# Kernel optimization log

Hardware: AMD Instinct MI355X
Metric: run time of the kernel (lower is better)

The kernel has to match this reference:

```python
import jax, jax.numpy as jnp
import numpy as np

N = 20000
E = 640000
IN_DIM = 128
HID = 128
OUT = 64


def setup_inputs() -> dict:
    key = jax.random.key(0)
    ks = jax.random.split(key, 16)
    s = 0.05
    inp = {
        'feat': jax.random.normal(ks[0], (N, IN_DIM), jnp.float32),
        'edge_index': jax.random.randint(ks[1], (2, E), 0, N, jnp.int64),
        # GCNConv params
        'W_gcn': jax.random.normal(ks[2], (IN_DIM, HID), jnp.float32) * s,
        'b_gcn': jnp.zeros((HID,), jnp.float32),
        # SAGEConv params (lin_l: aggregated neighbors w/ bias; lin_r: root, no bias)
        'W_sage_l': jax.random.normal(ks[3], (HID, HID), jnp.float32) * s,
        'b_sage_l': jnp.zeros((HID,), jnp.float32),
        'W_sage_r': jax.random.normal(ks[4], (HID, HID), jnp.float32) * s,
        # policy MLP
        'W1': jax.random.normal(ks[5], (HID, HID), jnp.float32) * s,
        'b1': jnp.zeros((HID,), jnp.float32),
        'W2': jax.random.normal(ks[6], (HID, HID), jnp.float32) * s,
        'b2': jnp.zeros((HID,), jnp.float32),
        'W3': jax.random.normal(ks[7], (HID, OUT), jnp.float32) * s,
        'b3': jnp.zeros((OUT,), jnp.float32),
        # value head
        'Wv': jax.random.normal(ks[8], (HID, 1), jnp.float32) * s,
        'bv': jnp.zeros((1,), jnp.float32),
    }
    return inp


def _gcn(feat, src, dst, W, b):
    # PyG GCNConv: add self loops, sym-normalize by deg^-1/2 on both ends
    loop = jnp.arange(N, dtype=src.dtype)
    s = jnp.concatenate([src, loop])
    d = jnp.concatenate([dst, loop])
    deg = jax.ops.segment_sum(jnp.ones_like(d, jnp.float32), d, num_segments=N)
    dinv = jnp.where(deg > 0, jax.lax.rsqrt(deg), 0.0)
    x = feat @ W  # [N, HID]
    msg = x[s] * (dinv[s] * dinv[d])[:, None]  # [E+N, HID]
    return jax.ops.segment_sum(msg, d, num_segments=N) + b


def _sage_mean(h, src, dst, Wl, bl, Wr):
    # PyG SAGEConv(aggr='mean'): lin_l(mean_neigh) + lin_r(root)
    neigh_sum = jax.ops.segment_sum(h[src], dst, num_segments=N)
    cnt = jax.ops.segment_sum(jnp.ones_like(dst, jnp.float32), dst, num_segments=N)
    mean = neigh_sum / jnp.maximum(cnt, 1.0)[:, None]
    return mean @ Wl + bl + h @ Wr


def reference(feat, edge_index, W_gcn, b_gcn, W_sage_l, b_sage_l, W_sage_r,
              W1, b1, W2, b2, W3, b3, Wv, bv):
    src, dst = edge_index[0], edge_index[1]
    h = jax.nn.relu(_gcn(feat, src, dst, W_gcn, b_gcn))
    h = jax.nn.relu(_sage_mean(h, src, dst, W_sage_l, b_sage_l, W_sage_r))
    # policy MLP (GELU exact, matching torch nn.GELU default)
    z = jax.nn.gelu(h @ W1 + b1, approximate=False)
    z = jax.nn.gelu(z @ W2 + b2, approximate=False)
    means = z @ W3 + b3  # [N, OUT]
    values = (h @ Wv + bv)[:, 0]  # [N]
    return (means, values)
```

## Files before the change

kernel.cpp:

```cpp
#include <hip/hip_runtime.h>
#include <math.h>


typedef __attribute__((ext_vector_type(8))) short short8;
typedef __attribute__((ext_vector_type(4))) float floatx4;

__device__ __forceinline__ unsigned short f2b(float f) {
    unsigned u = __float_as_uint(f);
    unsigned r = (u + 0x7fffu + ((u >> 16) & 1u)) >> 16;
    return (unsigned short)r;
}
__device__ __forceinline__ float b2f_lo(unsigned v) {
    return __uint_as_float(v << 16);
}
__device__ __forceinline__ float b2f_hi(unsigned v) {
    return __uint_as_float(v & 0xffff0000u);
}
__device__ __forceinline__ floatx4 MFMA(short8 a, short8 b, floatx4 c) {
    return __builtin_amdgcn_mfma_f32_16x16x32_bf16(a, b, c, 0, 0, 0);
}
__device__ __forceinline__ float gelu_exact(float x) {
    return 0.5f * x * (1.0f + erff(x * 0.70710678118654752440f));
}

#define FRAG(P, ct, ks, lane) (*(const short8*)((P) + (((((ct)*4 + (ks))*64) + (lane)) << 3)))


__global__ __launch_bounds__(256) void count_pack_kernel(
    const int* __restrict__ eidx, int E, int* __restrict__ cnt,
    const float* Wg, const float* Wsl, const float* Wsr,
    const float* W1, const float* W2, const float* W3,
    unsigned short* Pg, unsigned short* Psl, unsigned short* Psr,
    unsigned short* P1, unsigned short* P2, unsigned short* P3,
    int countBlocks)
{
    if ((int)blockIdx.x < countBlocks) {
        int e = blockIdx.x * 256 + threadIdx.x;
        if (e < E) atomicAdd(&cnt[eidx[E + e]], 1);
        return;
    }
    int t = (blockIdx.x - countBlocks) * 256 + threadIdx.x;
    const float* W; unsigned short* P; int NC = 128; int base;
    if (t < 2048)       { W = Wg;  P = Pg;  base = t; }
    else if (t < 4096)  { W = Wsl; P = Psl; base = t - 2048; }
    else if (t < 6144)  { W = Wsr; P = Psr; base = t - 4096; }
    else if (t < 8192)  { W = W1;  P = P1;  base = t - 6144; }
    else if (t < 10240) { W = W2;  P = P2;  base = t - 8192; }
    else if (t < 11264) { W = W3;  P = P3;  base = t - 10240; NC = 64; }
    else return;
    int l  = base & 63;
    int ks = (base >> 6) & 3;
    int ct = base >> 8;
    int n  = ct * 16 + (l & 15);
    int k0 = ks * 32 + ((l >> 4) << 3);
    short8 v;
    #pragma unroll
    for (int j = 0; j < 8; j++) v[j] = (short)f2b(W[(size_t)(k0 + j) * NC + n]);
    *(short8*)(P + ((size_t)base << 3)) = v;
}


__global__ __launch_bounds__(256) void scan_kernel(
    const int* __restrict__ cnt, int N,
    int* __restrict__ row_ptr, int* __restrict__ wptr, float* __restrict__ dinv,
    int* __restrict__ gflags, int* __restrict__ gsums)
{
    __shared__ int sh[256];
    __shared__ int s_off;
    int b = blockIdx.x, tid = threadIdx.x;
    int i0 = b * 1024 + tid * 4;
    int v0 = (i0 + 0 < N) ? cnt[i0 + 0] : 0;
    int v1 = (i0 + 1 < N) ? cnt[i0 + 1] : 0;
    int v2 = (i0 + 2 < N) ? cnt[i0 + 2] : 0;
    int v3 = (i0 + 3 < N) ? cnt[i0 + 3] : 0;
    int tot = v0 + v1 + v2 + v3;
    sh[tid] = tot;
    __syncthreads();
    for (int off = 1; off < 256; off <<= 1) {
        int t = (tid >= off) ? sh[tid - off] : 0;
        __syncthreads();
        sh[tid] += t;
        __syncthreads();
    }
    if (tid == 255) {
        gsums[b] = sh[255];
        __hip_atomic_store(&gflags[b], 1, __ATOMIC_RELEASE, __HIP_MEMORY_SCOPE_AGENT);
    }
    if (tid == 0) {
        int off = 0;
        for (int j = 0; j < b; j++) {
            while (__hip_atomic_load(&gflags[j], __ATOMIC_ACQUIRE,
                                     __HIP_MEMORY_SCOPE_AGENT) == 0) {}
            off += gsums[j];
        }
        s_off = off;
    }
    __syncthreads();
    int excl = s_off + sh[tid] - tot;
    if (i0 + 0 < N) { row_ptr[i0 + 0] = excl;                wptr[i0 + 0] = excl;                dinv[i0 + 0] = rsqrtf((float)(v0 + 1)); }
    if (i0 + 1 < N) { row_ptr[i0 + 1] = excl + v0;           wptr[i0 + 1] = excl + v0;           dinv[i0 + 1] = rsqrtf((float)(v1 + 1)); }
    if (i0 + 2 < N) { row_ptr[i0 + 2] = excl + v0 + v1;      wptr[i0 + 2] = excl + v0 + v1;      dinv[i0 + 2] = rsqrtf((float)(v2 + 1)); }
    if (i0 + 3 < N) { row_ptr[i0 + 3] = excl + v0 + v1 + v2; wptr[i0 + 3] = excl + v0 + v1 + v2; dinv[i0 + 3] = rsqrtf((float)(v3 + 1)); }
    if (b == (int)gridDim.x - 1 && tid == 255) row_ptr[N] = s_off + sh[255];
}


__global__ __launch_bounds__(256) void fill_gemm_kernel(
    const int* __restrict__ eidx, int E, int N,
    int* __restrict__ wptr, int* __restrict__ col,
    const float* __restrict__ feat, const float* __restrict__ dinv,
    const unsigned short* __restrict__ Pg, unsigned short* __restrict__ xs,
    int M, int fillBlocks, int PS)
{
    if ((int)blockIdx.x < fillBlocks) {
        int p = blockIdx.x & 7;
        int chunk = blockIdx.x >> 3;
        int dlo = p * PS;
        int dhi = dlo + PS; if (dhi > N) dhi = N;
        #pragma unroll
        for (int it = 0; it < 8; it++) {
            int e = (chunk * 8 + it) * 256 + threadIdx.x;
            if (e < E) {
                int d = eidx[E + e];
                if (d >= dlo && d < dhi) {
                    int pos = atomicAdd(&wptr[d], 1);
                    col[pos] = eidx[e];
                }
            }
        }
        return;
    }
    int bid = blockIdx.x - fillBlocks;
    int w = bid * 4 + (threadIdx.x >> 6);
    if (w >= (M / 16) * 2) return;
    int lane = threadIdx.x & 63;
    int m = lane & 15, quad = lane >> 4;
    int rt = w >> 1, ch = w & 1;
    const float* arow = feat + (size_t)(rt * 16 + m) * 128;
    short8 a[4];
    #pragma unroll
    for (int ks = 0; ks < 4; ks++) {
        float4 f0 = *(const float4*)(arow + ks * 32 + quad * 8);
        float4 f1 = *(const float4*)(arow + ks * 32 + quad * 8 + 4);
        short8 s;
        s[0] = (short)f2b(f0.x); s[1] = (short)f2b(f0.y);
        s[2] = (short)f2b(f0.z); s[3] = (short)f2b(f0.w);
        s[4] = (short)f2b(f1.x); s[5] = (short)f2b(f1.y);
        s[6] = (short)f2b(f1.z); s[7] = (short)f2b(f1.w);
        a[ks] = s;
    }
    float dvr[4];
    #pragma unroll
    for (int reg = 0; reg < 4; reg++) dvr[reg] = dinv[rt * 16 + quad * 4 + reg];
    #pragma unroll
    for (int ct = 0; ct < 4; ct++) {
        floatx4 acc = {0.f, 0.f, 0.f, 0.f};
        #pragma unroll
        for (int ks = 0; ks < 4; ks++)
            acc = MFMA(a[ks], FRAG(Pg, ch * 4 + ct, ks, lane), acc);
        #pragma unroll
        for (int reg = 0; reg < 4; reg++)
            xs[(size_t)(rt * 16 + quad * 4 + reg) * 128 + (ch * 4 + ct) * 16 + m] =
                f2b(acc[reg] * dvr[reg]);
    }
}


#define ACCUM(q)                                   \
    acc[0] += b2f_lo((q).x); acc[1] += b2f_hi((q).x); \
    acc[2] += b2f_lo((q).y); acc[3] += b2f_hi((q).y); \
    acc[4] += b2f_lo((q).z); acc[5] += b2f_hi((q).z); \
    acc[6] += b2f_lo((q).w); acc[7] += b2f_hi((q).w);

template<bool GCN>
__global__ __launch_bounds__(256) void agg_kernel(
    const unsigned short* __restrict__ X, const int* __restrict__ row_ptr,
    const int* __restrict__ col, const float* __restrict__ dinv,
    const float* __restrict__ bias, unsigned short* __restrict__ Y, int N)
{
    int w = (int)((blockIdx.x * 256 + threadIdx.x) >> 6);
    if (w >= N) return;
    int lane = threadIdx.x & 63;
    int g = lane >> 4, t = lane & 15;
    const uint4* Xq = (const uint4*)X;
    int beg = row_ptr[w], end = row_ptr[w + 1];
    int deg = end - beg;

    float acc[8] = {0.f, 0.f, 0.f, 0.f, 0.f, 0.f, 0.f, 0.f};
    int jb = beg;
    for (; jb + 16 <= end; jb += 16) {
        int s0 = col[jb + g];
        int s1 = col[jb + g + 4];
        int s2 = col[jb + g + 8];
        int s3 = col[jb + g + 12];
        uint4 q0 = Xq[(size_t)s0 * 16 + t];
        uint4 q1 = Xq[(size_t)s1 * 16 + t];
        uint4 q2 = Xq[(size_t)s2 * 16 + t];
        uint4 q3 = Xq[(size_t)s3 * 16 + t];
        ACCUM(q0) ACCUM(q1) ACCUM(q2) ACCUM(q3)
    }
    for (; jb < end; jb += 4) {
        int j = jb + g;
        if (j < end) {
            int s = col[j];
            uint4 q = Xq[(size_t)s * 16 + t];
            ACCUM(q)
        }
    }
    #pragma unroll
    for (int i = 0; i < 8; i++) {
        acc[i] += __shfl_xor(acc[i], 16);
        acc[i] += __shfl_xor(acc[i], 32);
    }
    if (g == 0) {
        float out[8];
        if (GCN) {
            uint4 q = Xq[(size_t)w * 16 + t];
            ACCUM(q)
            float dw = dinv[w];
            float4 b0 = *(const float4*)(bias + t * 8);
            float4 b1 = *(const float4*)(bias + t * 8 + 4);
            out[0] = fmaxf(fmaf(acc[0], dw, b0.x), 0.f);
            out[1] = fmaxf(fmaf(acc[1], dw, b0.y), 0.f);
            out[2] = fmaxf(fmaf(acc[2], dw, b0.z), 0.f);
            out[3] = fmaxf(fmaf(acc[3], dw, b0.w), 0.f);
            out[4] = fmaxf(fmaf(acc[4], dw, b1.x), 0.f);
            out[5] = fmaxf(fmaf(acc[5], dw, b1.y), 0.f);
            out[6] = fmaxf(fmaf(acc[6], dw, b1.z), 0.f);
            out[7] = fmaxf(fmaf(acc[7], dw, b1.w), 0.f);
        } else {
            float rc = 1.0f / (float)(deg > 0 ? deg : 1);
            #pragma unroll
            for (int i = 0; i < 8; i++) out[i] = acc[i] * rc;
        }
        uint4 r;
        r.x = (unsigned)f2b(out[0]) | ((unsigned)f2b(out[1]) << 16);
        r.y = (unsigned)f2b(out[2]) | ((unsigned)f2b(out[3]) << 16);
        r.z = (unsigned)f2b(out[4]) | ((unsigned)f2b(out[5]) << 16);
        r.w = (unsigned)f2b(out[6]) | ((unsigned)f2b(out[7]) << 16);
        ((uint4*)Y)[(size_t)w * 16 + t] = r;
    }
}


__global__ __launch_bounds__(256) void sage_mlp_kernel(
    const unsigned short* __restrict__ mean, const unsigned short* __restrict__ h1,
    const unsigned short* __restrict__ Psl, const unsigned short* __restrict__ Psr,
    const float* __restrict__ bsl,
    const unsigned short* __restrict__ P1, const float* __restrict__ b1,
    const unsigned short* __restrict__ P2, const float* __restrict__ b2,
    const unsigned short* __restrict__ P3, const float* __restrict__ b3,
    const float* __restrict__ Wv, const float* __restrict__ bv,
    float* __restrict__ means, float* __restrict__ values, int M)
{
    __shared__ unsigned short z[4][16 * 136];
    int widx = threadIdx.x >> 6, lane = threadIdx.x & 63;
    int w = blockIdx.x * 4 + widx;
    if (w >= M / 16) return;
    int m = lane & 15, quad = lane >> 4;
    unsigned short* zt = &z[widx][0];
    int r0 = w * 16;

    short8 am[4], ar[4];
    #pragma unroll
    for (int ks = 0; ks < 4; ks++) {
        am[ks] = *(const short8*)(mean + (size_t)(r0 + m) * 128 + ks * 32 + quad * 8);
        ar[ks] = *(const short8*)(h1   + (size_t)(r0 + m) * 128 + ks * 32 + quad * 8);
    }

    float vpart[4] = {0.f, 0.f, 0.f, 0.f};
    #pragma unroll
    for (int ct = 0; ct < 8; ct++) {
        floatx4 acc = {0.f, 0.f, 0.f, 0.f};
        #pragma unroll
        for (int ks = 0; ks < 4; ks++) acc = MFMA(am[ks], FRAG(Psl, ct, ks, lane), acc);
        #pragma unroll
        for (int ks = 0; ks < 4; ks++) acc = MFMA(ar[ks], FRAG(Psr, ct, ks, lane), acc);
        float bb = bsl[ct * 16 + m];
        float wv = Wv[ct * 16 + m];
        #pragma unroll
        for (int reg = 0; reg < 4; reg++) {
            float o = fmaxf(acc[reg] + bb, 0.f);
            vpart[reg] = fmaf(o, wv, vpart[reg]);
            zt[(quad * 4 + reg) * 136 + ct * 16 + m] = f2b(o);
        }
    }
    #pragma unroll
    for (int off = 1; off <= 8; off <<= 1) {
        #pragma unroll
        for (int reg = 0; reg < 4; reg++)
            vpart[reg] += __shfl_xor(vpart[reg], off);
    }
    if (m == 0) {
        float bvv = bv[0];
        #pragma unroll
        for (int reg = 0; reg < 4; reg++)
            values[r0 + quad * 4 + reg] = vpart[reg] + bvv;
    }

    short8 a1[4];
    #pragma unroll
    for (int ks = 0; ks < 4; ks++)
        a1[ks] = *(const short8*)(zt + m * 136 + ks * 32 + quad * 8);

    #pragma unroll
    for (int ct = 0; ct < 8; ct++) {
        floatx4 acc = {0.f, 0.f, 0.f, 0.f};
        #pragma unroll
        for (int ks = 0; ks < 4; ks++) acc = MFMA(a1[ks], FRAG(P1, ct, ks, lane), acc);
        float bb = b1[ct * 16 + m];
        #pragma unroll
        for (int reg = 0; reg < 4; reg++)
            zt[(quad * 4 + reg) * 136 + ct * 16 + m] = f2b(gelu_exact(acc[reg] + bb));
    }
    short8 a2[4];
    #pragma unroll
    for (int ks = 0; ks < 4; ks++)
        a2[ks] = *(const short8*)(zt + m * 136 + ks * 32 + quad * 8);

    #pragma unroll
    for (int ct = 0; ct < 8; ct++) {
        floatx4 acc = {0.f, 0.f, 0.f, 0.f};
        #pragma unroll
        for (int ks = 0; ks < 4; ks++) acc = MFMA(a2[ks], FRAG(P2, ct, ks, lane), acc);
        float bb = b2[ct * 16 + m];
        #pragma unroll
        for (int reg = 0; reg < 4; reg++)
            zt[(quad * 4 + reg) * 136 + ct * 16 + m] = f2b(gelu_exact(acc[reg] + bb));
    }
    short8 a3[4];
    #pragma unroll
    for (int ks = 0; ks < 4; ks++)
        a3[ks] = *(const short8*)(zt + m * 136 + ks * 32 + quad * 8);

    #pragma unroll
    for (int ct = 0; ct < 4; ct++) {
        floatx4 acc = {0.f, 0.f, 0.f, 0.f};
        #pragma unroll
        for (int ks = 0; ks < 4; ks++) acc = MFMA(a3[ks], FRAG(P3, ct, ks, lane), acc);
        float bb = b3[ct * 16 + m];
        #pragma unroll
        for (int reg = 0; reg < 4; reg++)
            means[(size_t)(r0 + quad * 4 + reg) * 64 + ct * 16 + m] = acc[reg] + bb;
    }
}


extern "C" void kernel_launch(void* const* d_in, const int* in_sizes, int n_in,
                              void* d_out, int out_size, void* d_ws, size_t ws_size,
                              hipStream_t stream) {
    const float* feat  = (const float*)d_in[0];
    const int*   eidx  = (const int*)d_in[1];
    const float* W_gcn = (const float*)d_in[2];
    const float* b_gcn = (const float*)d_in[3];
    const float* W_sl  = (const float*)d_in[4];
    const float* b_sl  = (const float*)d_in[5];
    const float* W_sr  = (const float*)d_in[6];
    const float* W1    = (const float*)d_in[7];
    const float* b1    = (const float*)d_in[8];
    const float* W2    = (const float*)d_in[9];
    const float* b2    = (const float*)d_in[10];
    const float* W3    = (const float*)d_in[11];
    const float* b3    = (const float*)d_in[12];
    const float* Wv    = (const float*)d_in[13];
    const float* bv    = (const float*)d_in[14];

    const int N = in_sizes[0] / 128;
    const int E = in_sizes[1] / 2;

    char* ws = (char*)d_ws;
    size_t off = 0;
    auto alloc = [&](size_t bytes) -> void* {
        void* p = ws + off;
        off += (bytes + 255) & ~(size_t)255;
        return p;
    };
    int*   gflags  = (int*)alloc((size_t)(64 + N) * 4);
    int*   cnt     = gflags + 64;
    size_t zbytes  = (size_t)(64 + N) * 4;
    int*   gsums   = (int*)alloc(64 * 4);
    int*   row_ptr = (int*)alloc((size_t)(N + 1) * 4);
    int*   wptr    = (int*)alloc((size_t)N * 4);
    float* dinv    = (float*)alloc((size_t)N * 4);
    int*   col     = (int*)alloc((size_t)E * 4);
    unsigned short* xs   = (unsigned short*)alloc((size_t)N * 128 * 2);
    unsigned short* h1   = (unsigned short*)alloc((size_t)N * 128 * 2);
    unsigned short* mean = (unsigned short*)alloc((size_t)N * 128 * 2);
    unsigned short* Pg   = (unsigned short*)alloc(2048 * 8 * 2);
    unsigned short* Psl  = (unsigned short*)alloc(2048 * 8 * 2);
    unsigned short* Psr  = (unsigned short*)alloc(2048 * 8 * 2);
    unsigned short* P1   = (unsigned short*)alloc(2048 * 8 * 2);
    unsigned short* P2   = (unsigned short*)alloc(2048 * 8 * 2);
    unsigned short* P3   = (unsigned short*)alloc(1024 * 8 * 2);

    hipMemsetAsync(gflags, 0, zbytes, stream);

    const int countBlocks = (E + 255) / 256;
    const int packBlocks  = (11264 + 255) / 256;
    count_pack_kernel<<<countBlocks + packBlocks, 256, 0, stream>>>(
        eidx, E, cnt, W_gcn, W_sl, W_sr, W1, W2, W3,
        Pg, Psl, Psr, P1, P2, P3, countBlocks);

    const int NB = (N + 1023) / 1024;
    scan_kernel<<<NB, 256, 0, stream>>>(cnt, N, row_ptr, wptr, dinv, gflags, gsums);

    const int PS = (N + 7) / 8;
    const int chunks = (E + 2047) / 2048;
    const int fillBlocks = chunks * 8;
    const int gemmBlocks = ((N / 16) * 2 + 3) / 4;
    fill_gemm_kernel<<<fillBlocks + gemmBlocks, 256, 0, stream>>>(
        eidx, E, N, wptr, col, feat, dinv, Pg, xs, N, fillBlocks, PS);

    const int agrid = (N + 3) / 4;
    agg_kernel<true><<<agrid, 256, 0, stream>>>(xs, row_ptr, col, dinv, b_gcn, h1, N);
    agg_kernel<false><<<agrid, 256, 0, stream>>>(h1, row_ptr, col, dinv, nullptr, mean, N);

    sage_mlp_kernel<<<(N / 16 + 3) / 4, 256, 0, stream>>>(
        mean, h1, Psl, Psr, b_sl, P1, b1, P2, b2, P3, b3, Wv, bv,
        (float*)d_out, (float*)d_out + (size_t)N * 64, N);
}
```

Measured before the change: 221.0 us.

## Record per-edge rank during counting and restructure aggregation to two nodes per wave

Result: slower. 253.7 us (+14.8%).

```diff
diff --git a/kernel.cpp b/kernel.cpp
--- a/kernel.cpp
+++ b/kernel.cpp
@@ -7,27 +7,25 @@
 
 __device__ __forceinline__ unsigned short f2b(float f) {
     unsigned u = __float_as_uint(f);
-    unsigned r = (u + 0x7fffu + ((u >> 16) & 1u)) >> 16;
-    return (unsigned short)r;
-}
-__device__ __forceinline__ float b2f_lo(unsigned v) {
-    return __uint_as_float(v << 16);
-}
-__device__ __forceinline__ float b2f_hi(unsigned v) {
-    return __uint_as_float(v & 0xffff0000u);
-}
+    return (unsigned short)((u + 0x7fffu + ((u >> 16) & 1u)) >> 16);
+}
+__device__ __forceinline__ unsigned pack2(float a, float b) {
+    return (unsigned)f2b(a) | ((unsigned)f2b(b) << 16);
+}
+__device__ __forceinline__ float b2f_lo(unsigned v) { return __uint_as_float(v << 16); }
+__device__ __forceinline__ float b2f_hi(unsigned v) { return __uint_as_float(v & 0xffff0000u); }
 __device__ __forceinline__ floatx4 MFMA(short8 a, short8 b, floatx4 c) {
     return __builtin_amdgcn_mfma_f32_16x16x32_bf16(a, b, c, 0, 0, 0);
 }
 __device__ __forceinline__ float gelu_exact(float x) {
     return 0.5f * x * (1.0f + erff(x * 0.70710678118654752440f));
 }
-
 #define FRAG(P, ct, ks, lane) (*(const short8*)((P) + (((((ct)*4 + (ks))*64) + (lane)) << 3)))
 
 
 __global__ __launch_bounds__(256) void count_pack_kernel(
-    const int* __restrict__ eidx, int E, int* __restrict__ cnt,
+    const int* __restrict__ eidx, int E,
+    int* __restrict__ cnt, int* __restrict__ rank,
     const float* Wg, const float* Wsl, const float* Wsr,
     const float* W1, const float* W2, const float* W3,
     unsigned short* Pg, unsigned short* Psl, unsigned short* Psr,
@@ -36,7 +34,10 @@
 {
     if ((int)blockIdx.x < countBlocks) {
         int e = blockIdx.x * 256 + threadIdx.x;
-        if (e < E) atomicAdd(&cnt[eidx[E + e]], 1);
+        if (e < E) {
+            int d = eidx[E + e];
+            rank[e] = atomicAdd(&cnt[d], 1);
+        }
         return;
     }
     int t = (blockIdx.x - countBlocks) * 256 + threadIdx.x;
@@ -62,7 +63,7 @@
 
 __global__ __launch_bounds__(256) void scan_kernel(
     const int* __restrict__ cnt, int N,
-    int* __restrict__ row_ptr, int* __restrict__ wptr, float* __restrict__ dinv,
+    int* __restrict__ row_ptr, float* __restrict__ dinv,
     int* __restrict__ gflags, int* __restrict__ gsums)
 {
     __shared__ int sh[256];
@@ -97,36 +98,27 @@
     }
     __syncthreads();
     int excl = s_off + sh[tid] - tot;
-    if (i0 + 0 < N) { row_ptr[i0 + 0] = excl;                wptr[i0 + 0] = excl;                dinv[i0 + 0] = rsqrtf((float)(v0 + 1)); }
-    if (i0 + 1 < N) { row_ptr[i0 + 1] = excl + v0;           wptr[i0 + 1] = excl + v0;           dinv[i0 + 1] = rsqrtf((float)(v1 + 1)); }
-    if (i0 + 2 < N) { row_ptr[i0 + 2] = excl + v0 + v1;      wptr[i0 + 2] = excl + v0 + v1;      dinv[i0 + 2] = rsqrtf((float)(v2 + 1)); }
-    if (i0 + 3 < N) { row_ptr[i0 + 3] = excl + v0 + v1 + v2; wptr[i0 + 3] = excl + v0 + v1 + v2; dinv[i0 + 3] = rsqrtf((float)(v3 + 1)); }
+    if (i0 + 0 < N) { row_ptr[i0 + 0] = excl;                dinv[i0 + 0] = rsqrtf((float)(v0 + 1)); }
+    if (i0 + 1 < N) { row_ptr[i0 + 1] = excl + v0;           dinv[i0 + 1] = rsqrtf((float)(v1 + 1)); }
+    if (i0 + 2 < N) { row_ptr[i0 + 2] = excl + v0 + v1;      dinv[i0 + 2] = rsqrtf((float)(v2 + 1)); }
+    if (i0 + 3 < N) { row_ptr[i0 + 3] = excl + v0 + v1 + v2; dinv[i0 + 3] = rsqrtf((float)(v3 + 1)); }
     if (b == (int)gridDim.x - 1 && tid == 255) row_ptr[N] = s_off + sh[255];
 }
 
 
 __global__ __launch_bounds__(256) void fill_gemm_kernel(
-    const int* __restrict__ eidx, int E, int N,
-    int* __restrict__ wptr, int* __restrict__ col,
+    const int* __restrict__ eidx, const int* __restrict__ rank,
+    const int* __restrict__ row_ptr, int E, int* __restrict__ col,
     const float* __restrict__ feat, const float* __restrict__ dinv,
     const unsigned short* __restrict__ Pg, unsigned short* __restrict__ xs,
-    int M, int fillBlocks, int PS)
+    int M, int fillBlocks)
 {
     if ((int)blockIdx.x < fillBlocks) {
-        int p = blockIdx.x & 7;
-        int chunk = blockIdx.x >> 3;
-        int dlo = p * PS;
-        int dhi = dlo + PS; if (dhi > N) dhi = N;
-        #pragma unroll
-        for (int it = 0; it < 8; it++) {
-            int e = (chunk * 8 + it) * 256 + threadIdx.x;
-            if (e < E) {
-                int d = eidx[E + e];
-                if (d >= dlo && d < dhi) {
-                    int pos = atomicAdd(&wptr[d], 1);
-                    col[pos] = eidx[e];
-                }
-            }
+        int e = blockIdx.x * 256 + threadIdx.x;
+        if (e < E) {
+            int d = eidx[E + e];
+            int pos = row_ptr[d] + rank[e];
+            __builtin_nontemporal_store(eidx[e], &col[pos]);
         }
         return;
     }
@@ -166,11 +158,12 @@
 }
 
 
-#define ACCUM(q)                                   \
-    acc[0] += b2f_lo((q).x); acc[1] += b2f_hi((q).x); \
-    acc[2] += b2f_lo((q).y); acc[3] += b2f_hi((q).y); \
-    acc[4] += b2f_lo((q).z); acc[5] += b2f_hi((q).z); \
-    acc[6] += b2f_lo((q).w); acc[7] += b2f_hi((q).w);
+__device__ __forceinline__ void acc8(float* a, uint4 q) {
+    a[0] += b2f_lo(q.x); a[1] += b2f_hi(q.x);
+    a[2] += b2f_lo(q.y); a[3] += b2f_hi(q.y);
+    a[4] += b2f_lo(q.z); a[5] += b2f_hi(q.z);
+    a[6] += b2f_lo(q.w); a[7] += b2f_hi(q.w);
+}
 
 template<bool GCN>
 __global__ __launch_bounds__(256) void agg_kernel(
@@ -178,67 +171,114 @@
     const int* __restrict__ col, const float* __restrict__ dinv,
     const float* __restrict__ bias, unsigned short* __restrict__ Y, int N)
 {
-    int w = (int)((blockIdx.x * 256 + threadIdx.x) >> 6);
-    if (w >= N) return;
+    int pw = (int)((blockIdx.x * 256 + threadIdx.x) >> 6);
+    if (pw * 2 >= N) return;
     int lane = threadIdx.x & 63;
-    int g = lane >> 4, t = lane & 15;
+    int t = lane & 7, g = lane >> 3;
     const uint4* Xq = (const uint4*)X;
-    int beg = row_ptr[w], end = row_ptr[w + 1];
-    int deg = end - beg;
-
-    float acc[8] = {0.f, 0.f, 0.f, 0.f, 0.f, 0.f, 0.f, 0.f};
-    int jb = beg;
-    for (; jb + 16 <= end; jb += 16) {
-        int s0 = col[jb + g];
-        int s1 = col[jb + g + 4];
-        int s2 = col[jb + g + 8];
-        int s3 = col[jb + g + 12];
-        uint4 q0 = Xq[(size_t)s0 * 16 + t];
-        uint4 q1 = Xq[(size_t)s1 * 16 + t];
-        uint4 q2 = Xq[(size_t)s2 * 16 + t];
-        uint4 q3 = Xq[(size_t)s3 * 16 + t];
-        ACCUM(q0) ACCUM(q1) ACCUM(q2) ACCUM(q3)
-    }
-    for (; jb < end; jb += 4) {
-        int j = jb + g;
-        if (j < end) {
-            int s = col[j];
-            uint4 q = Xq[(size_t)s * 16 + t];
-            ACCUM(q)
-        }
-    }
-    #pragma unroll
-    for (int i = 0; i < 8; i++) {
-        acc[i] += __shfl_xor(acc[i], 16);
-        acc[i] += __shfl_xor(acc[i], 32);
-    }
-    if (g == 0) {
-        float out[8];
-        if (GCN) {
-            uint4 q = Xq[(size_t)w * 16 + t];
-            ACCUM(q)
-            float dw = dinv[w];
-            float4 b0 = *(const float4*)(bias + t * 8);
-            float4 b1 = *(const float4*)(bias + t * 8 + 4);
-            out[0] = fmaxf(fmaf(acc[0], dw, b0.x), 0.f);
-            out[1] = fmaxf(fmaf(acc[1], dw, b0.y), 0.f);
-            out[2] = fmaxf(fmaf(acc[2], dw, b0.z), 0.f);
-            out[3] = fmaxf(fmaf(acc[3], dw, b0.w), 0.f);
-            out[4] = fmaxf(fmaf(acc[4], dw, b1.x), 0.f);
-            out[5] = fmaxf(fmaf(acc[5], dw, b1.y), 0.f);
-            out[6] = fmaxf(fmaf(acc[6], dw, b1.z), 0.f);
-            out[7] = fmaxf(fmaf(acc[7], dw, b1.w), 0.f);
-        } else {
-            float rc = 1.0f / (float)(deg > 0 ? deg : 1);
-            #pragma unroll
-            for (int i = 0; i < 8; i++) out[i] = acc[i] * rc;
-        }
-        uint4 r;
-        r.x = (unsigned)f2b(out[0]) | ((unsigned)f2b(out[1]) << 16);
-        r.y = (unsigned)f2b(out[2]) | ((unsigned)f2b(out[3]) << 16);
-        r.z = (unsigned)f2b(out[4]) | ((unsigned)f2b(out[5]) << 16);
-        r.w = (unsigned)f2b(out[6]) | ((unsigned)f2b(out[7]) << 16);
-        ((uint4*)Y)[(size_t)w * 16 + t] = r;
+    int w0 = pw * 2, w1 = w0 + 1;
+    int beg0 = row_ptr[w0];
+    int mid  = row_ptr[w1];
+    int end1 = row_ptr[w1 + 1];
+
+    #pragma unroll
+    for (int half = 0; half < 2; half++) {
+        const int hoff = half * 8;
+        float a0[8] = {0.f,0.f,0.f,0.f,0.f,0.f,0.f,0.f};
+        float a1[8] = {0.f,0.f,0.f,0.f,0.f,0.f,0.f,0.f};
+        int jb0 = beg0, jb1 = mid;
+        while (jb0 + 32 <= mid && jb1 + 32 <= end1) {
+            int s00 = __builtin_nontemporal_load(&col[jb0 + g]);
+            int s01 = __builtin_nontemporal_load(&col[jb0 + 8 + g]);
+            int s02 = __builtin_nontemporal_load(&col[jb0 + 16 + g]);
+            int s03 = __builtin_nontemporal_load(&col[jb0 + 24 + g]);
+            int s10 = __builtin_nontemporal_load(&col[jb1 + g]);
+            int s11 = __builtin_nontemporal_load(&col[jb1 + 8 + g]);
+            int s12 = __builtin_nontemporal_load(&col[jb1 + 16 + g]);
+            int s13 = __builtin_nontemporal_load(&col[jb1 + 24 + g]);
+            uint4 q00 = Xq[(size_t)s00 * 16 + hoff + t];
+            uint4 q01 = Xq[(size_t)s01 * 16 + hoff + t];
+            uint4 q02 = Xq[(size_t)s02 * 16 + hoff + t];
+            uint4 q03 = Xq[(size_t)s03 * 16 + hoff + t];
+            uint4 q10 = Xq[(size_t)s10 * 16 + hoff + t];
+            uint4 q11 = Xq[(size_t)s11 * 16 + hoff + t];
+            uint4 q12 = Xq[(size_t)s12 * 16 + hoff + t];
+            uint4 q13 = Xq[(size_t)s13 * 16 + hoff + t];
+            acc8(a0, q00); acc8(a0, q01); acc8(a0, q02); acc8(a0, q03);
+            acc8(a1, q10); acc8(a1, q11); acc8(a1, q12); acc8(a1, q13);
+            jb0 += 32; jb1 += 32;
+        }
+        while (jb0 + 32 <= mid) {
+            int s0 = __builtin_nontemporal_load(&col[jb0 + g]);
+            int s1 = __builtin_nontemporal_load(&col[jb0 + 8 + g]);
+            int s2 = __builtin_nontemporal_load(&col[jb0 + 16 + g]);
+            int s3 = __builtin_nontemporal_load(&col[jb0 + 24 + g]);
+            uint4 q0 = Xq[(size_t)s0 * 16 + hoff + t];
+            uint4 q1 = Xq[(size_t)s1 * 16 + hoff + t];
+            uint4 q2 = Xq[(size_t)s2 * 16 + hoff + t];
+            uint4 q3 = Xq[(size_t)s3 * 16 + hoff + t];
+            acc8(a0, q0); acc8(a0, q1); acc8(a0, q2); acc8(a0, q3);
+            jb0 += 32;
+        }
+        while (jb1 + 32 <= end1) {
+            int s0 = __builtin_nontemporal_load(&col[jb1 + g]);
+            int s1 = __builtin_nontemporal_load(&col[jb1 + 8 + g]);
+            int s2 = __builtin_nontemporal_load(&col[jb1 + 16 + g]);
+            int s3 = __builtin_nontemporal_load(&col[jb1 + 24 + g]);
+            uint4 q0 = Xq[(size_t)s0 * 16 + hoff + t];
+            uint4 q1 = Xq[(size_t)s1 * 16 + hoff + t];
+            uint4 q2 = Xq[(size_t)s2 * 16 + hoff + t];
+            uint4 q3 = Xq[(size_t)s3 * 16 + hoff + t];
+            acc8(a1, q0); acc8(a1, q1); acc8(a1, q2); acc8(a1, q3);
+            jb1 += 32;
+        }
+        for (int j = jb0 + g; j < mid; j += 8) {
+            int s = __builtin_nontemporal_load(&col[j]);
+            uint4 q = Xq[(size_t)s * 16 + hoff + t];
+            acc8(a0, q);
+        }
+        for (int j = jb1 + g; j < end1; j += 8) {
+            int s = __builtin_nontemporal_load(&col[j]);
+            uint4 q = Xq[(size_t)s * 16 + hoff + t];
+            acc8(a1, q);
+        }
+        #pragma unroll
+        for (int i = 0; i < 8; i++) {
+            a0[i] += __shfl_xor(a0[i], 8);  a1[i] += __shfl_xor(a1[i], 8);
+            a0[i] += __shfl_xor(a0[i], 16); a1[i] += __shfl_xor(a1[i], 16);
+            a0[i] += __shfl_xor(a0[i], 32); a1[i] += __shfl_xor(a1[i], 32);
+        }
+        int w = (g == 0) ? w0 : w1;
+        float* a = (g == 0) ? a0 : a1;
+        int deg = (g == 0) ? (mid - beg0) : (end1 - mid);
+        if (g < 2) {
+            float out[8];
+            if (GCN) {
+                uint4 q = Xq[(size_t)w * 16 + hoff + t];
+                acc8(a, q);
+                float dw = dinv[w];
+                float4 b0 = *(const float4*)(bias + half * 64 + t * 8);
+                float4 b1 = *(const float4*)(bias + half * 64 + t * 8 + 4);
+                out[0] = fmaxf(fmaf(a[0], dw, b0.x), 0.f);
+                out[1] = fmaxf(fmaf(a[1], dw, b0.y), 0.f);
+                out[2] = fmaxf(fmaf(a[2], dw, b0.z), 0.f);
+                out[3] = fmaxf(fmaf(a[3], dw, b0.w), 0.f);
+                out[4] = fmaxf(fmaf(a[4], dw, b1.x), 0.f);
+                out[5] = fmaxf(fmaf(a[5], dw, b1.y), 0.f);
+                out[6] = fmaxf(fmaf(a[6], dw, b1.z), 0.f);
+                out[7] = fmaxf(fmaf(a[7], dw, b1.w), 0.f);
+            } else {
+                float rc = 1.0f / (float)(deg > 0 ? deg : 1);
+                #pragma unroll
+                for (int i = 0; i < 8; i++) out[i] = a[i] * rc;
+            }
+            uint4 r;
+            r.x = pack2(out[0], out[1]);
+            r.y = pack2(out[2], out[3]);
+            r.z = pack2(out[4], out[5]);
+            r.w = pack2(out[6], out[7]);
+            ((uint4*)Y)[(size_t)w * 16 + hoff + t] = r;
+        }
     }
 }
 
@@ -379,8 +419,8 @@
     int*   cnt     = gflags + 64;
     size_t zbytes  = (size_t)(64 + N) * 4;
     int*   gsums   = (int*)alloc(64 * 4);
+    int*   rank    = (int*)alloc((size_t)E * 4);
     int*   row_ptr = (int*)alloc((size_t)(N + 1) * 4);
-    int*   wptr    = (int*)alloc((size_t)N * 4);
     float* dinv    = (float*)alloc((size_t)N * 4);
     int*   col     = (int*)alloc((size_t)E * 4);
     unsigned short* xs   = (unsigned short*)alloc((size_t)N * 128 * 2);
@@ -389,33 +429,31 @@
     unsigned short* Pg   = (unsigned short*)alloc(2048 * 8 * 2);
     unsigned short* Psl  = (unsigned short*)alloc(2048 * 8 * 2);
     unsigned short* Psr  = (unsigned short*)alloc(2048 * 8 * 2);
-    unsigned short* P1   = (unsigned short*)alloc(2048 * 8 * 2);
-    unsigned short* P2   = (unsigned short*)alloc(2048 * 8 * 2);
-    unsigned short* P3   = (unsigned short*)alloc(1024 * 8 * 2);
+    unsigned short* P1p  = (unsigned short*)alloc(2048 * 8 * 2);
+    unsigned short* P2p  = (unsigned short*)alloc(2048 * 8 * 2);
+    unsigned short* P3p  = (unsigned short*)alloc(1024 * 8 * 2);
 
     hipMemsetAsync(gflags, 0, zbytes, stream);
 
     const int countBlocks = (E + 255) / 256;
     const int packBlocks  = (11264 + 255) / 256;
     count_pack_kernel<<<countBlocks + packBlocks, 256, 0, stream>>>(
-        eidx, E, cnt, W_gcn, W_sl, W_sr, W1, W2, W3,
-        Pg, Psl, Psr, P1, P2, P3, countBlocks);
+        eidx, E, cnt, rank, W_gcn, W_sl, W_sr, W1, W2, W3,
+        Pg, Psl, Psr, P1p, P2p, P3p, countBlocks);
 
     const int NB = (N + 1023) / 1024;
-    scan_kernel<<<NB, 256, 0, stream>>>(cnt, N, row_ptr, wptr, dinv, gflags, gsums);
-
-    const int PS = (N + 7) / 8;
-    const int chunks = (E + 2047) / 2048;
-    const int fillBlocks = chunks * 8;
+    scan_kernel<<<NB, 256, 0, stream>>>(cnt, N, row_ptr, dinv, gflags, gsums);
+
+    const int fillBlocks = (E + 255) / 256;
     const int gemmBlocks = ((N / 16) * 2 + 3) / 4;
     fill_gemm_kernel<<<fillBlocks + gemmBlocks, 256, 0, stream>>>(
-        eidx, E, N, wptr, col, feat, dinv, Pg, xs, N, fillBlocks, PS);
-
-    const int agrid = (N + 3) / 4;
+        eidx, rank, row_ptr, E, col, feat, dinv, Pg, xs, N, fillBlocks);
+
+    const int agrid = ((N + 1) / 2 + 3) / 4;
     agg_kernel<true><<<agrid, 256, 0, stream>>>(xs, row_ptr, col, dinv, b_gcn, h1, N);
     agg_kernel<false><<<agrid, 256, 0, stream>>>(h1, row_ptr, col, dinv, nullptr, mean, N);
 
     sage_mlp_kernel<<<(N / 16 + 3) / 4, 256, 0, stream>>>(
-        mean, h1, Psl, Psr, b_sl, P1, b1, P2, b2, P3, b3, Wv, bv,
+        mean, h1, Psl, Psr, b_sl, P1p, b1, P2p, b2, P3p, b3, Wv, bv,
         (float*)d_out, (float*)d_out + (size_t)N * 64, N);
 }
```
